# Optimization experiments

Measured on AMD Instinct MI355X. Metric: run time of the kernel, lower is better.

The kernel has to match this reference:

```python
import jax, jax.numpy as jnp
from jax import lax
import numpy as np

MEM_SZ = 1024
SOMA_FAST = 4.0
SOMA_SLOW = 7.0
MOD_BIAS = 0.4
EPS_BASE = 0.9
BIAS_MOD_RANGE = 5.0


def setup_inputs() -> dict:
    key = jax.random.key(0)
    k1, k2, k3 = jax.random.split(key, 3)
    B, L, IN = 128, 512, 512
    u = jax.random.normal(k1, (B, L, IN), dtype=jnp.float32)
    h0 = jnp.zeros((2, B, MEM_SZ), dtype=jnp.float32)
    W_im = jax.random.normal(k2, (2 * MEM_SZ, IN), dtype=jnp.float32) * 0.05
    b_im = jax.random.normal(k3, (2 * MEM_SZ,), dtype=jnp.float32) * 0.05
    return {"u": u, "h0": h0, "W_im": W_im, "b_im": b_im}


def reference(u, h0, W_im, b_im):
    # Hoisted input projection: one big GEMM over all timesteps.
    # in_emb: [B, L, 2*mem]
    in_emb = jnp.einsum('bli,oi->blo', u, W_im) + b_im
    c1 = in_emb[..., :MEM_SZ]          # soma_bias_contribution_1
    i_o = in_emb[..., MEM_SZ:]
    soma_bias = jnp.tanh(c1 / BIAS_MOD_RANGE) * BIAS_MOD_RANGE

    def step(carry, inp):
        hf, hs = carry
        sb, io = inp
        hfn = jnp.tanh(io + SOMA_FAST * hf
                       - SOMA_SLOW * jnp.square(hs + MOD_BIAS) + sb)
        # variable_eps: 0.9 + 0.9 / (1 + exp((hf - 0.5) / -0.1))
        eps = EPS_BASE + EPS_BASE * jax.nn.sigmoid((hf - 0.5) * 10.0)
        hsn = (1.0 - eps) * hs + eps * hf
        return (hfn, hsn), hfn

    # scan over time: inputs as [L, B, mem]
    xs = (jnp.transpose(soma_bias, (1, 0, 2)), jnp.transpose(i_o, (1, 0, 2)))
    (hf_last, _hs_last), hf_seq = lax.scan(step, (h0[0], h0[1]), xs)
    h_t = jnp.transpose(hf_seq, (1, 0, 2))  # [B, L, mem]
    return h_t, hf_last
```

## Files before the change

### kernel.cpp

```cpp
#include <hip/hip_runtime.h>
#include <hip/hip_fp16.h>

#define MEM  1024
#define B_   128
#define L_   512
#define M_   (B_*L_)
#define N_   (2*MEM)
#define K_   512

#define SCALE_U 16.0f
#define SCALE_W 1024.0f
#define INV_SCALE (1.0f / (16.0f * 1024.0f))

typedef __attribute__((ext_vector_type(8))) _Float16 half8;
typedef __attribute__((ext_vector_type(4))) float f32x4;

__device__ __forceinline__ float fast_tanh(float x) {
    float e = __expf(2.0f * x);
    return 1.0f - 2.0f / (e + 1.0f);
}
__device__ __forceinline__ float fast_sigmoid(float x) {
    return 1.0f / (1.0f + __expf(-x));
}
__device__ __forceinline__ void gl_lds16(const void* g, void* l) {
    __builtin_amdgcn_global_load_lds(
        (const __attribute__((address_space(1))) void*)g,
        (__attribute__((address_space(3))) void*)l, 16, 0, 0);
}

__global__ void split_fp32_fp16x2(const float* __restrict__ in,
                                  unsigned short* __restrict__ hi,
                                  unsigned short* __restrict__ lo,
                                  int n4, float scale) {
    int i = blockIdx.x * 256 + threadIdx.x;
    if (i >= n4) return;
    const float4 v = reinterpret_cast<const float4*>(in)[i];
    float vs[4] = {v.x, v.y, v.z, v.w};
    unsigned short hs_[4], ls_[4];
#pragma unroll
    for (int c = 0; c < 4; ++c) {
        float xs = vs[c] * scale;
        __half h = __float2half_rn(xs);
        float r = xs - __half2float(h);
        __half l = __float2half_rn(r);
        hs_[c] = __half_as_ushort(h);
        ls_[c] = __half_as_ushort(l);
    }
    ushort4 h4, l4;
    h4.x = hs_[0]; h4.y = hs_[1]; h4.z = hs_[2]; h4.w = hs_[3];
    l4.x = ls_[0]; l4.y = ls_[1]; l4.z = ls_[2]; l4.w = ls_[3];
    reinterpret_cast<ushort4*>(hi)[i] = h4;
    reinterpret_cast<ushort4*>(lo)[i] = l4;
}

#define TM 128
#define TN 128
#define BK 32
__global__ __launch_bounds__(256, 2) void gemm_paired_kernel(
    const unsigned short* __restrict__ uh, const unsigned short* __restrict__ ul,
    const unsigned short* __restrict__ wh, const unsigned short* __restrict__ wl,
    const float* __restrict__ bias,
    float* __restrict__ z_out) {
    __shared__ __attribute__((aligned(16))) unsigned short Ah[TM * BK];
    __shared__ __attribute__((aligned(16))) unsigned short Al[TM * BK];
    __shared__ __attribute__((aligned(16))) unsigned short Bh0[TN * BK];
    __shared__ __attribute__((aligned(16))) unsigned short Bl0[TN * BK];
    __shared__ __attribute__((aligned(16))) unsigned short Bh1[TN * BK];
    __shared__ __attribute__((aligned(16))) unsigned short Bl1[TN * BK];

    const int tid = threadIdx.x;
    const int id  = blockIdx.x;
    const int mt  = (id >> 6) * 8 + (id & 7);
    const int nt  = (id >> 3) & 7;
    const int tileM = mt * TM;
    const int tileN = nt * TN;

    const int lane = tid & 63, w = tid >> 6;
    const int wm = w & 1, wn = w >> 1;
    const int lrow = lane & 15, quad = lane >> 4;
    const int q2 = quad ^ ((lrow >> 1) & 3);

    f32x4 acc0[4][4] = {};
    f32x4 acc1[4][4] = {};

    const int i0 = tid, i1 = tid + 256;
    const int r0 = i0 >> 2, gs0 = (i0 & 3) ^ ((r0 >> 1) & 3);
    const int r1 = i1 >> 2, gs1 = (i1 & 3) ^ ((r1 >> 1) & 3);
    const size_t sA0 = (size_t)(tileM + r0) * K_ + gs0 * 8;
    const size_t sA1 = (size_t)(tileM + r1) * K_ + gs1 * 8;
    const size_t sB0a = (size_t)(tileN + r0) * K_ + gs0 * 8;
    const size_t sB0b = (size_t)(tileN + r1) * K_ + gs1 * 8;
    const size_t sB1a = (size_t)(tileN + 1024 + r0) * K_ + gs0 * 8;
    const size_t sB1b = (size_t)(tileN + 1024 + r1) * K_ + gs1 * 8;

    for (int kt = 0; kt < K_ / BK; ++kt) {
        const size_t ko = (size_t)kt * BK;
        __syncthreads();
        gl_lds16(uh + sA0 + ko, &Ah[i0 * 8]);
        gl_lds16(uh + sA1 + ko, &Ah[i1 * 8]);
        gl_lds16(ul + sA0 + ko, &Al[i0 * 8]);
        gl_lds16(ul + sA1 + ko, &Al[i1 * 8]);
        gl_lds16(wh + sB0a + ko, &Bh0[i0 * 8]);
        gl_lds16(wh + sB0b + ko, &Bh0[i1 * 8]);
        gl_lds16(wl + sB0a + ko, &Bl0[i0 * 8]);
        gl_lds16(wl + sB0b + ko, &Bl0[i1 * 8]);
        gl_lds16(wh + sB1a + ko, &Bh1[i0 * 8]);
        gl_lds16(wh + sB1b + ko, &Bh1[i1 * 8]);
        gl_lds16(wl + sB1a + ko, &Bl1[i0 * 8]);
        gl_lds16(wl + sB1b + ko, &Bl1[i1 * 8]);
        __syncthreads();

        half8 ahf[4], alf[4];
#pragma unroll
        for (int i = 0; i < 4; ++i) {
            const int ao = ((wm * 64 + i * 16 + lrow) * 4 + q2) * 8;
            ahf[i] = *(const half8*)&Ah[ao];
            alf[i] = *(const half8*)&Al[ao];
        }
#pragma unroll
        for (int j = 0; j < 4; ++j) {
            const int bo = ((wn * 64 + j * 16 + lrow) * 4 + q2) * 8;
            const half8 b0h = *(const half8*)&Bh0[bo];
            const half8 b0l = *(const half8*)&Bl0[bo];
            const half8 b1h = *(const half8*)&Bh1[bo];
            const half8 b1l = *(const half8*)&Bl1[bo];
#pragma unroll
            for (int i = 0; i < 4; ++i) {
                f32x4 c0 = acc0[i][j];
                c0 = __builtin_amdgcn_mfma_f32_16x16x32_f16(ahf[i], b0h, c0, 0, 0, 0);
                c0 = __builtin_amdgcn_mfma_f32_16x16x32_f16(ahf[i], b0l, c0, 0, 0, 0);
                c0 = __builtin_amdgcn_mfma_f32_16x16x32_f16(alf[i], b0h, c0, 0, 0, 0);
                acc0[i][j] = c0;
                f32x4 c1 = acc1[i][j];
                c1 = __builtin_amdgcn_mfma_f32_16x16x32_f16(ahf[i], b1h, c1, 0, 0, 0);
                c1 = __builtin_amdgcn_mfma_f32_16x16x32_f16(ahf[i], b1l, c1, 0, 0, 0);
                c1 = __builtin_amdgcn_mfma_f32_16x16x32_f16(alf[i], b1h, c1, 0, 0, 0);
                acc1[i][j] = c1;
            }
        }
    }

#pragma unroll
    for (int j = 0; j < 4; ++j) {
        const int c = tileN + wn * 64 + j * 16 + lrow;
        const float b1v = bias[c];
        const float b2v = bias[c + 1024];
#pragma unroll
        for (int i = 0; i < 4; ++i) {
            const int rowb = tileM + wm * 64 + i * 16 + quad * 4;
#pragma unroll
            for (int r = 0; r < 4; ++r) {
                float v1 = acc0[i][j][r] * INV_SCALE + b1v;
                v1 = fast_tanh(v1 * 0.2f) * 5.0f;
                const float v2 = acc1[i][j][r] * INV_SCALE + b2v;
                z_out[(size_t)(rowb + r) * MEM + c] = v1 + v2;
            }
        }
    }
}

__global__ __launch_bounds__(256) void scan_kernel(
    const float* __restrict__ z,
    float* __restrict__ h_t,
    const float* __restrict__ h0,
    float* __restrict__ hf_last) {
    const int idx = blockIdx.x * 256 + threadIdx.x;
    const int b = idx >> 10, m = idx & (MEM - 1);
    float hf = h0[idx];
    float hs = h0[B_ * MEM + idx];
    const size_t base = (size_t)b * L_ * MEM + m;

    float zv[4];
#pragma unroll
    for (int j = 0; j < 4; ++j) zv[j] = z[base + (size_t)j * MEM];

    for (int l0 = 0; l0 < L_; l0 += 4) {
        float zn[4];
        const bool more = (l0 + 4) < L_;
        if (more) {
#pragma unroll
            for (int j = 0; j < 4; ++j)
                zn[j] = z[base + (size_t)(l0 + 4 + j) * MEM];
        }
#pragma unroll
        for (int j = 0; j < 4; ++j) {
            const float hsb = hs + 0.4f;
            const float x = zv[j] + 4.0f * hf - 7.0f * hsb * hsb;
            const float hfn = fast_tanh(x);
            const float eps = 0.9f + 0.9f * fast_sigmoid(10.0f * (hf - 0.5f));
            hs = hs + eps * (hf - hs);
            h_t[base + (size_t)(l0 + j) * MEM] = hfn;
            hf = hfn;
        }
        if (more) {
#pragma unroll
            for (int j = 0; j < 4; ++j) zv[j] = zn[j];
        }
    }
    hf_last[idx] = hf;
}

extern "C" void kernel_launch(void* const* d_in, const int* in_sizes, int n_in,
                              void* d_out, int out_size, void* d_ws, size_t ws_size,
                              hipStream_t stream) {
    const float* u    = (const float*)d_in[0];
    const float* h0   = (const float*)d_in[1];
    const float* W_im = (const float*)d_in[2];
    const float* b_im = (const float*)d_in[3];

    float* out = (float*)d_out;
    float* h_t = out;
    float* hf_last = out + (size_t)M_ * MEM;

    char* ws = (char*)d_ws;
    float* z           = (float*)ws;
    unsigned short* uh = (unsigned short*)(ws + 268435456ull);
    unsigned short* ul = (unsigned short*)(ws + 335544320ull);
    unsigned short* wh = (unsigned short*)(ws + 402653184ull);
    unsigned short* wl = (unsigned short*)(ws + 404750336ull);

    {
        const int n4_u = (M_ * K_) / 4;
        const int n4_w = (N_ * K_) / 4;
        split_fp32_fp16x2<<<(n4_u + 255) / 256, 256, 0, stream>>>(u, uh, ul, n4_u, SCALE_U);
        split_fp32_fp16x2<<<(n4_w + 255) / 256, 256, 0, stream>>>(W_im, wh, wl, n4_w, SCALE_W);
    }
    {
        gemm_paired_kernel<<<4096, 256, 0, stream>>>(uh, ul, wh, wl, b_im, z);
    }
    {
        scan_kernel<<<(B_ * MEM) / 256, 256, 0, stream>>>(z, h_t, h0, hf_last);
    }
}
```

Baseline: 863.8 us.

## Fuse fp32-to-fp16x2 split of u into GEMM A-tile load; deepen scan prefetch

Drops the separate pass that split the 128MB input u into hi/lo fp16 arrays. The GEMM now loads fp32 u tiles directly into LDS with an XOR swizzle and does the hi/lo split in registers before the MFMAs. This avoids writing and re-reading about 128MB of intermediates, at the cost of more LDS traffic per A tile, extra conversion work in the inner loop, and more register pressure. The scan kernel also prefetches 16 timesteps of z ahead instead of 4, to hide more memory latency.

```diff
diff --git a/kernel.cpp b/kernel.cpp
--- a/kernel.cpp
+++ b/kernel.cpp
@@ -57,12 +57,11 @@
 #define TN 128
 #define BK 32
 __global__ __launch_bounds__(256, 2) void gemm_paired_kernel(
-    const unsigned short* __restrict__ uh, const unsigned short* __restrict__ ul,
+    const float* __restrict__ u,
     const unsigned short* __restrict__ wh, const unsigned short* __restrict__ wl,
     const float* __restrict__ bias,
     float* __restrict__ z_out) {
-    __shared__ __attribute__((aligned(16))) unsigned short Ah[TM * BK];
-    __shared__ __attribute__((aligned(16))) unsigned short Al[TM * BK];
+    __shared__ __attribute__((aligned(16))) float Af[TM * BK];
     __shared__ __attribute__((aligned(16))) unsigned short Bh0[TN * BK];
     __shared__ __attribute__((aligned(16))) unsigned short Bl0[TN * BK];
     __shared__ __attribute__((aligned(16))) unsigned short Bh1[TN * BK];
@@ -83,11 +82,17 @@
     f32x4 acc0[4][4] = {};
     f32x4 acc1[4][4] = {};
 
+    size_t aoff[4];
+#pragma unroll
+    for (int c = 0; c < 4; ++c) {
+        const int p = c * 256 + tid;
+        const int row = p >> 3;
+        const int chunk = (p & 7) ^ (row & 7);
+        aoff[c] = (size_t)(tileM + row) * K_ + chunk * 4;
+    }
     const int i0 = tid, i1 = tid + 256;
     const int r0 = i0 >> 2, gs0 = (i0 & 3) ^ ((r0 >> 1) & 3);
     const int r1 = i1 >> 2, gs1 = (i1 & 3) ^ ((r1 >> 1) & 3);
-    const size_t sA0 = (size_t)(tileM + r0) * K_ + gs0 * 8;
-    const size_t sA1 = (size_t)(tileM + r1) * K_ + gs1 * 8;
     const size_t sB0a = (size_t)(tileN + r0) * K_ + gs0 * 8;
     const size_t sB0b = (size_t)(tileN + r1) * K_ + gs1 * 8;
     const size_t sB1a = (size_t)(tileN + 1024 + r0) * K_ + gs0 * 8;
@@ -96,10 +101,9 @@
     for (int kt = 0; kt < K_ / BK; ++kt) {
         const size_t ko = (size_t)kt * BK;
         __syncthreads();
-        gl_lds16(uh + sA0 + ko, &Ah[i0 * 8]);
-        gl_lds16(uh + sA1 + ko, &Ah[i1 * 8]);
-        gl_lds16(ul + sA0 + ko, &Al[i0 * 8]);
-        gl_lds16(ul + sA1 + ko, &Al[i1 * 8]);
+#pragma unroll
+        for (int c = 0; c < 4; ++c)
+            gl_lds16(u + aoff[c] + ko, &Af[c * 1024 + tid * 4]);
         gl_lds16(wh + sB0a + ko, &Bh0[i0 * 8]);
         gl_lds16(wh + sB0b + ko, &Bh0[i1 * 8]);
         gl_lds16(wl + sB0a + ko, &Bl0[i0 * 8]);
@@ -113,9 +117,23 @@
         half8 ahf[4], alf[4];
 #pragma unroll
         for (int i = 0; i < 4; ++i) {
-            const int ao = ((wm * 64 + i * 16 + lrow) * 4 + q2) * 8;
-            ahf[i] = *(const half8*)&Ah[ao];
-            alf[i] = *(const half8*)&Al[ao];
+            const int r = wm * 64 + i * 16 + lrow;
+            const int sw = r & 7;
+            const f32x4 t0 = *(const f32x4*)&Af[(r * 8 + ((quad * 2)     ^ sw)) * 4];
+            const f32x4 t1 = *(const f32x4*)&Af[(r * 8 + ((quad * 2 + 1) ^ sw)) * 4];
+            half8 h, l;
+#pragma unroll
+            for (int e = 0; e < 4; ++e) {
+                float xs = t0[e] * SCALE_U;
+                _Float16 hh = (_Float16)xs;
+                h[e] = hh;
+                l[e] = (_Float16)(xs - (float)hh);
+                xs = t1[e] * SCALE_U;
+                hh = (_Float16)xs;
+                h[e + 4] = hh;
+                l[e + 4] = (_Float16)(xs - (float)hh);
+            }
+            ahf[i] = h; alf[i] = l;
         }
 #pragma unroll
         for (int j = 0; j < 4; ++j) {
@@ -170,20 +188,19 @@
     float hs = h0[B_ * MEM + idx];
     const size_t base = (size_t)b * L_ * MEM + m;
 
-    float zv[4];
-#pragma unroll
-    for (int j = 0; j < 4; ++j) zv[j] = z[base + (size_t)j * MEM];
-
-    for (int l0 = 0; l0 < L_; l0 += 4) {
-        float zn[4];
-        const bool more = (l0 + 4) < L_;
+    float zv[16], zn[16];
+#pragma unroll
+    for (int j = 0; j < 16; ++j) zv[j] = z[base + (size_t)j * MEM];
+
+    for (int l0 = 0; l0 < L_; l0 += 16) {
+        const bool more = (l0 + 16) < L_;
         if (more) {
 #pragma unroll
-            for (int j = 0; j < 4; ++j)
-                zn[j] = z[base + (size_t)(l0 + 4 + j) * MEM];
-        }
-#pragma unroll
-        for (int j = 0; j < 4; ++j) {
+            for (int j = 0; j < 16; ++j)
+                zn[j] = z[base + (size_t)(l0 + 16 + j) * MEM];
+        }
+#pragma unroll
+        for (int j = 0; j < 16; ++j) {
             const float hsb = hs + 0.4f;
             const float x = zv[j] + 4.0f * hf - 7.0f * hsb * hsb;
             const float hfn = fast_tanh(x);
@@ -194,7 +211,7 @@
         }
         if (more) {
 #pragma unroll
-            for (int j = 0; j < 4; ++j) zv[j] = zn[j];
+            for (int j = 0; j < 16; ++j) zv[j] = zn[j];
         }
     }
     hf_last[idx] = hf;
@@ -214,19 +231,15 @@
 
     char* ws = (char*)d_ws;
     float* z           = (float*)ws;
-    unsigned short* uh = (unsigned short*)(ws + 268435456ull);
-    unsigned short* ul = (unsigned short*)(ws + 335544320ull);
-    unsigned short* wh = (unsigned short*)(ws + 402653184ull);
-    unsigned short* wl = (unsigned short*)(ws + 404750336ull);
+    unsigned short* wh = (unsigned short*)(ws + 268435456ull);
+    unsigned short* wl = (unsigned short*)(ws + 270532608ull);
 
     {
-        const int n4_u = (M_ * K_) / 4;
         const int n4_w = (N_ * K_) / 4;
-        split_fp32_fp16x2<<<(n4_u + 255) / 256, 256, 0, stream>>>(u, uh, ul, n4_u, SCALE_U);
         split_fp32_fp16x2<<<(n4_w + 255) / 256, 256, 0, stream>>>(W_im, wh, wl, n4_w, SCALE_W);
     }
     {
-        gemm_paired_kernel<<<4096, 256, 0, stream>>>(uh, ul, wh, wl, b_im, z);
+        gemm_paired_kernel<<<4096, 256, 0, stream>>>(u, wh, wl, b_im, z);
     }
     {
         scan_kernel<<<(B_ * MEM) / 256, 256, 0, stream>>>(z, h_t, h0, hf_last);
```

New measurement: 781.5 us. 9.5% less time.
